# Kernel optimization log

Hardware: AMD Instinct MI355X
Metric: run time of the kernel (lower is better)

## Reference

```python
import jax, jax.numpy as jnp
import numpy as np

N_NODES = 100000
N_EDGES = 600000
NODE_DIM = 64
EDGE_DIM = 32
HID = 128
OUT = 24


def setup_inputs() -> dict:
    key = jax.random.key(0)
    ks = jax.random.split(key, 20)

    def w(k, shape):
        return jax.random.normal(k, shape, jnp.float32) * (1.0 / np.sqrt(shape[0]).astype(np.float32))

    inp = {}
    inp["x"] = jax.random.normal(ks[0], (N_NODES, NODE_DIM), jnp.float32)
    inp["edge_index"] = jax.random.randint(ks[1], (2, N_EDGES), 0, N_NODES)
    inp["edge_attr"] = jax.random.normal(ks[2], (N_EDGES, EDGE_DIM), jnp.float32)
    inp["lin1_w"] = w(ks[3], (NODE_DIM, HID)); inp["lin1_b"] = jnp.zeros((HID,), jnp.float32)
    i = 4
    for c in (1, 2, 3):
        inp[f"conv{c}_edge_w"] = w(ks[i], (EDGE_DIM, HID)); inp[f"conv{c}_edge_b"] = jnp.zeros((HID,), jnp.float32)
        inp[f"conv{c}_w1"] = w(ks[i + 1], (HID, HID)); inp[f"conv{c}_b1"] = jnp.zeros((HID,), jnp.float32)
        inp[f"conv{c}_w2"] = w(ks[i + 2], (HID, HID)); inp[f"conv{c}_b2"] = jnp.zeros((HID,), jnp.float32)
        i += 3
    inp["cls_w1"] = w(ks[i], (2 * HID + EDGE_DIM, HID)); inp["cls_b1"] = jnp.zeros((HID,), jnp.float32)
    inp["cls_w2"] = w(ks[i + 1], (HID, OUT)); inp["cls_b2"] = jnp.zeros((OUT,), jnp.float32)
    return inp


def _gine(h, src, dst, e_emb, w1, b1, w2, b2, eps=0.0):
    # GINEConv: out = MLP((1+eps)*x + sum_{j->i} relu(x_j + edge_emb))
    m = jax.nn.relu(h[src] + e_emb)                       # [E, HID] gather + fuse
    agg = jax.ops.segment_sum(m, dst, num_segments=N_NODES)  # scatter-add to dst
    z = (1.0 + eps) * h + agg
    return jax.nn.relu(z @ w1 + b1) @ w2 + b2


def reference(x, edge_index, edge_attr,
              lin1_w, lin1_b,
              conv1_edge_w, conv1_edge_b, conv1_w1, conv1_b1, conv1_w2, conv1_b2,
              conv2_edge_w, conv2_edge_b, conv2_w1, conv2_b1, conv2_w2, conv2_b2,
              conv3_edge_w, conv3_edge_b, conv3_w1, conv3_b1, conv3_w2, conv3_b2,
              cls_w1, cls_b1, cls_w2, cls_b2):
    src, dst = edge_index[0], edge_index[1]
    h = x @ lin1_w + lin1_b                               # [N, HID]
    layers = [
        (conv1_edge_w, conv1_edge_b, conv1_w1, conv1_b1, conv1_w2, conv1_b2),
        (conv2_edge_w, conv2_edge_b, conv2_w1, conv2_b1, conv2_w2, conv2_b2),
        (conv3_edge_w, conv3_edge_b, conv3_w1, conv3_b1, conv3_w2, conv3_b2),
    ]
    for ew, eb, w1, b1, w2, b2 in layers:
        e_emb = edge_attr @ ew + eb                       # [E, HID]
        h = jax.nn.relu(_gine(h, src, dst, e_emb, w1, b1, w2, b2))
    edge_feat = jnp.concatenate([h[src], h[dst], edge_attr], axis=-1)  # [E, 2*HID+EDGE_DIM]
    return jax.nn.relu(edge_feat @ cls_w1 + cls_b1) @ cls_w2 + cls_b2  # [E, OUT]
```

## Files before the change

### kernel.cpp

```cpp
#include <hip/hip_runtime.h>

#define N_NODES 100000
#define N_EDGES 600000
#define NODE_DIM 64
#define EDGE_DIM 32
#define HID 128
#define OUT_DIM 24

typedef short short8 __attribute__((ext_vector_type(8)));
typedef short short4v __attribute__((ext_vector_type(4)));
typedef float f32x4 __attribute__((ext_vector_type(4)));

#define MFMA16(a, b, c) __builtin_amdgcn_mfma_f32_16x16x32_bf16(a, b, c, 0, 0, 0)

__device__ inline unsigned short f2bf(float f) {
  unsigned u = __float_as_uint(f);
  u += 0x7FFFu + ((u >> 16) & 1u);
  return (unsigned short)(u >> 16);
}
__device__ inline float bf2f(unsigned short b) {
  return __uint_as_float(((unsigned)b) << 16);
}

#define OFF_CW1T 0
#define OFF_CW2T 36864
#define OFF_LAYER(c) (40960 + (c)*65536)
#define OFF_EWT(c) (237568 + (c)*8192)
#define W_TOTAL 262144

__global__ __launch_bounds__(256) void prep_weights(
    const float* __restrict__ cw1, const float* __restrict__ cw2,
    const float* __restrict__ l0w1, const float* __restrict__ l0w2,
    const float* __restrict__ l1w1, const float* __restrict__ l1w2,
    const float* __restrict__ l2w1, const float* __restrict__ l2w2,
    const float* __restrict__ e0w, const float* __restrict__ e1w,
    const float* __restrict__ e2w,
    unsigned short* __restrict__ wb) {
  int i = blockIdx.x * 256 + threadIdx.x;
  if (i < 36864) {
    int n = i / 288, k = i % 288;
    wb[OFF_CW1T + i] = f2bf(cw1[k * 128 + n]);
  }
  int j = i - 36864;
  if (j >= 0 && j < 4096) {
    int n = j / 128, k = j % 128;
    wb[OFF_CW2T + j] = f2bf(n < 24 ? cw2[k * 24 + n] : 0.f);
  }
  int t = i - 40960;
  if (t >= 0 && t < 3 * 32768) {
    int c = t / 32768, u = t % 32768;
    const float* w = (u < 16384) ? (c == 0 ? l0w1 : c == 1 ? l1w1 : l2w1)
                                 : (c == 0 ? l0w2 : c == 1 ? l1w2 : l2w2);
    int v = u & 16383;
    int n = v >> 7, k = v & 127;
    float val = w[k * 128 + n];
    unsigned short hi = f2bf(val);
    unsigned short lo = f2bf(val - bf2f(hi));
    int base = OFF_LAYER(c) + (u < 16384 ? 0 : 32768);
    wb[base + v] = hi;
    wb[base + 16384 + v] = lo;
  }
  int p = i - 139264;
  if (p >= 0 && p < 3 * 8192) {
    int c = p / 8192, u = p % 8192;
    int v = u & 4095;
    int s = v >> 3, jj = v & 7;
    int ntile = s >> 6, kgrp = (s >> 4) & 3, nrow = s & 15;
    int n = ntile * 16 + nrow, k = kgrp * 8 + jj;
    const float* ew = (c == 0 ? e0w : c == 1 ? e1w : e2w);
    float val = ew[k * 128 + n];
    unsigned short hi = f2bf(val);
    wb[OFF_EWT(c) + u] = (u < 4096) ? hi : f2bf(val - bf2f(hi));
  }
}

__global__ __launch_bounds__(256) void lin1_kernel(
    const float* __restrict__ x, const float* __restrict__ w,
    const float* __restrict__ b, float* __restrict__ h,
    unsigned short* __restrict__ hbf) {
  __shared__ float4 smem4[3072];
  float* sA = (float*)smem4;
  float* sB = (float*)smem4 + 4096;
  int tid = threadIdx.x;
  int tn = tid & 31, tm = tid >> 5;
  int mbase = blockIdx.x * 64;

  for (int i = tid; i < 1024; i += 256) {
    int m = i & 63, k4 = (i >> 6) << 2;
    int row = mbase + m; if (row >= N_NODES) row = N_NODES - 1;
    float4 v = *(const float4*)(x + (size_t)row * NODE_DIM + k4);
    sA[(k4 + 0) * 64 + m] = v.x; sA[(k4 + 1) * 64 + m] = v.y;
    sA[(k4 + 2) * 64 + m] = v.z; sA[(k4 + 3) * 64 + m] = v.w;
  }
  for (int i = tid; i < 2048; i += 256)
    *(float4*)&sB[i * 4] = ((const float4*)w)[i];
  __syncthreads();

  float acc[8][4] = {};
#pragma unroll 8
  for (int k = 0; k < 64; ++k) {
    float4 a0 = *(float4*)&sA[k * 64 + tm * 8];
    float4 a1 = *(float4*)&sA[k * 64 + tm * 8 + 4];
    float4 bv = *(float4*)&sB[k * 128 + tn * 4];
    float av[8] = {a0.x, a0.y, a0.z, a0.w, a1.x, a1.y, a1.z, a1.w};
    float bb[4] = {bv.x, bv.y, bv.z, bv.w};
#pragma unroll
    for (int i = 0; i < 8; ++i)
#pragma unroll
      for (int jj = 0; jj < 4; ++jj) acc[i][jj] = fmaf(av[i], bb[jj], acc[i][jj]);
  }
  float4 bv = *(const float4*)(b + tn * 4);
#pragma unroll
  for (int i = 0; i < 8; ++i) {
    int row = mbase + tm * 8 + i;
    if (row < N_NODES) {
      float4 o = {acc[i][0] + bv.x, acc[i][1] + bv.y, acc[i][2] + bv.z, acc[i][3] + bv.w};
      *(float4*)(h + (size_t)row * HID + tn * 4) = o;
      short4v pk = {(short)f2bf(o.x), (short)f2bf(o.y), (short)f2bf(o.z), (short)f2bf(o.w)};
      *(short4v*)(hbf + (size_t)row * HID + tn * 4) = pk;
    }
  }
}

__global__ __launch_bounds__(256) void hist_kernel(
    const int* __restrict__ dst, int* __restrict__ counts) {
  int e = blockIdx.x * 256 + threadIdx.x;
  if (e < N_EDGES) atomicAdd(&counts[dst[e]], 1);
}

#define SCAN_BLK 98
__global__ __launch_bounds__(256) void scan_partial(
    const int* __restrict__ cnt, int* __restrict__ partial) {
  __shared__ int sdata[256];
  int b = blockIdx.x, t = threadIdx.x;
  int sum = 0;
  for (int i = t; i < 1024; i += 256) {
    int idx = b * 1024 + i;
    sum += (idx < N_NODES) ? cnt[idx] : 0;
  }
  sdata[t] = sum; __syncthreads();
  for (int s = 128; s > 0; s >>= 1) {
    if (t < s) sdata[t] += sdata[t + s];
    __syncthreads();
  }
  if (t == 0) partial[b] = sdata[0];
}

__global__ void scan_sums(const int* __restrict__ partial,
                          int* __restrict__ partialScan, int* __restrict__ rowptr) {
  if (threadIdx.x == 0) {
    int acc = 0;
    for (int i = 0; i < SCAN_BLK; ++i) { partialScan[i] = acc; acc += partial[i]; }
    rowptr[N_NODES] = acc;
  }
}

__global__ __launch_bounds__(256) void scan_final(
    const int* __restrict__ cnt, const int* __restrict__ partialScan,
    int* __restrict__ rowptr, int* __restrict__ cur) {
  __shared__ int sdata[256];
  int b = blockIdx.x, t = threadIdx.x;
  int i0 = b * 1024 + t * 4;
  int c[4]; int s = 0;
#pragma unroll
  for (int j = 0; j < 4; ++j) {
    c[j] = (i0 + j < N_NODES) ? cnt[i0 + j] : 0;
    s += c[j];
  }
  sdata[t] = s; __syncthreads();
  for (int d = 1; d < 256; d <<= 1) {
    int u = (t >= d) ? sdata[t - d] : 0;
    __syncthreads();
    sdata[t] += u;
    __syncthreads();
  }
  int off = sdata[t] - s + partialScan[b];
#pragma unroll
  for (int j = 0; j < 4; ++j) {
    int idx = i0 + j;
    if (idx < N_NODES) { rowptr[idx] = off; cur[idx] = off; off += c[j]; }
  }
}

__global__ __launch_bounds__(256) void scatter_kernel(
    const int* __restrict__ dst, const int* __restrict__ src,
    int* __restrict__ cur, int* __restrict__ perm,
    int* __restrict__ srcp, int* __restrict__ dstp) {
  int e = blockIdx.x * 256 + threadIdx.x;
  if (e < N_EDGES) {
    int d = dst[e];
    int slot = atomicAdd(&cur[d], 1);
    perm[slot] = e;
    srcp[slot] = src[e];
    dstp[slot] = d;
  }
}

__global__ __launch_bounds__(256) void build_eafrag(
    const float* __restrict__ ea, const int* __restrict__ perm,
    unsigned short* __restrict__ frag) {
  int slot = blockIdx.x * 256 + threadIdx.x;
  if (slot >= N_EDGES) return;
  int e = perm[slot];
  const float4* row = (const float4*)(ea + (size_t)e * EDGE_DIM);
  unsigned short* dp = frag + ((size_t)(slot >> 7)) * 4096 +
                       (size_t)(((slot & 127) >> 4)) * 512 + (slot & 15) * 8;
#pragma unroll
  for (int kg = 0; kg < 4; ++kg) {
    float4 v0 = row[kg * 2], v1 = row[kg * 2 + 1];
    short8 pk = {(short)f2bf(v0.x), (short)f2bf(v0.y), (short)f2bf(v0.z), (short)f2bf(v0.w),
                 (short)f2bf(v1.x), (short)f2bf(v1.y), (short)f2bf(v1.z), (short)f2bf(v1.w)};
    *(short8*)(dp + kg * 128) = pk;
  }
}

__global__ __launch_bounds__(256) void edge_agg_kernel(
    const unsigned short* __restrict__ hbf, const unsigned short* __restrict__ eafrag,
    const int* __restrict__ srcp, const int* __restrict__ dstp,
    const unsigned short* __restrict__ ewt, const float* __restrict__ eb,
    float* __restrict__ agg) {
  __shared__ float emb[128 * 132];
  __shared__ int sidx[128];
  __shared__ int sdst[128];
  int tid = threadIdx.x, lane = tid & 63, wave = tid >> 6;
  int wm = wave & 1, wn = wave >> 1;
  int sbase = blockIdx.x * 128;
  int nrows = N_EDGES - sbase; if (nrows > 128) nrows = 128;
  if (tid < 128) {
    int sl = sbase + tid;
    sidx[tid] = (sl < N_EDGES) ? srcp[sl] : 0;
    sdst[tid] = (sl < N_EDGES) ? dstp[sl] : -1;
  }
  const short8* Af = (const short8*)(eafrag) + (size_t)blockIdx.x * 512;
  const short8* Bh = (const short8*)(ewt);
  const short8* Bl = (const short8*)(ewt + 4096);
  short8 af[4], bh[4], bl[4];
#pragma unroll
  for (int mt = 0; mt < 4; ++mt) af[mt] = Af[(wm * 4 + mt) * 64 + lane];
#pragma unroll
  for (int nt = 0; nt < 4; ++nt) {
    bh[nt] = Bh[(wn * 4 + nt) * 64 + lane];
    bl[nt] = Bl[(wn * 4 + nt) * 64 + lane];
  }
  const f32x4 zf = {0.f, 0.f, 0.f, 0.f};
  f32x4 acc[4][4];
#pragma unroll
  for (int mt = 0; mt < 4; ++mt)
#pragma unroll
    for (int nt = 0; nt < 4; ++nt) {
      acc[mt][nt] = MFMA16(af[mt], bh[nt], zf);
      acc[mt][nt] = MFMA16(af[mt], bl[nt], acc[mt][nt]);
    }
  int q = lane >> 4, r = lane & 15;
#pragma unroll
  for (int nt = 0; nt < 4; ++nt) {
    int n = wn * 64 + nt * 16 + r;
    float ebv = eb[n];
#pragma unroll
    for (int mt = 0; mt < 4; ++mt) {
      int rowb = (wm * 4 + mt) * 16 + q * 4;
#pragma unroll
      for (int i2 = 0; i2 < 4; ++i2)
        emb[(rowb + i2) * 132 + n] = acc[mt][nt][i2] + ebv;
    }
  }
  __syncthreads();
  {
    int r0 = wave * 32;
    int cl = (lane & 31) * 4;
#pragma unroll 8
    for (int rr = 0; rr < 16; ++rr) {
      int row = r0 + rr * 2 + (lane >> 5);
      int s = sidx[row];
      uint2 u = *(const uint2*)(hbf + (size_t)s * HID + cl);
      float4 ev = *(float4*)(emb + row * 132 + cl);
      ev.x = fmaxf(ev.x + bf2f((unsigned short)u.x), 0.f);
      ev.y = fmaxf(ev.y + bf2f((unsigned short)(u.x >> 16)), 0.f);
      ev.z = fmaxf(ev.z + bf2f((unsigned short)u.y), 0.f);
      ev.w = fmaxf(ev.w + bf2f((unsigned short)(u.y >> 16)), 0.f);
      *(float4*)(emb + row * 132 + cl) = ev;
    }
  }
  __syncthreads();
  {
    int hh = tid >> 7;
    int col = tid & 127;
    int rbeg = hh * 64;
    int rend = rbeg + 64; if (rend > nrows) rend = nrows;
    if (rbeg < rend) {
      float a = 0.f;
      int cnode = sdst[rbeg];
      bool atomic_first = true;
      for (int rr = rbeg; rr < rend; ++rr) {
        int node = sdst[rr];
        if (node != cnode) {
          if (atomic_first) atomicAdd(&agg[(size_t)cnode * HID + col], a);
          else agg[(size_t)cnode * HID + col] = a;
          a = 0.f; cnode = node; atomic_first = false;
        }
        a += emb[rr * 132 + col];
      }
      atomicAdd(&agg[(size_t)cnode * HID + col], a);
    }
  }
}

__global__ __launch_bounds__(256) void agg_gather_kernel(
    const float* __restrict__ h, const float* __restrict__ ea,
    const int* __restrict__ srcp, const int* __restrict__ perm,
    const int* __restrict__ rowptr,
    const float* __restrict__ ew, const float* __restrict__ eb,
    float* __restrict__ agg) {
  int tid = threadIdx.x, lane = tid & 63;
  int wid = blockIdx.x * 4 + (tid >> 6);
  int nwaves = gridDim.x * 4;
  const float2* ew2 = (const float2*)ew;
  float2 ebv = *(const float2*)(eb + lane * 2);

  for (int node = wid; node < N_NODES; node += nwaves) {
    int beg = rowptr[node], end = rowptr[node + 1];
    float2 acc = {0.f, 0.f};
    for (int i = beg; i < end; ++i) {
      int s0 = srcp[i];
      int e0 = perm[i];
      float2 h0 = *(const float2*)(h + (size_t)s0 * HID + lane * 2);
      const float4* ea0 = (const float4*)(ea + (size_t)e0 * EDGE_DIM);
      float2 m0 = ebv;
#pragma unroll
      for (int k4 = 0; k4 < 8; ++k4) {
        float4 a0 = ea0[k4];
        float a0v[4] = {a0.x, a0.y, a0.z, a0.w};
#pragma unroll
        for (int j = 0; j < 4; ++j) {
          float2 w = ew2[(k4 * 4 + j) * 64 + lane];
          m0.x = fmaf(a0v[j], w.x, m0.x);
          m0.y = fmaf(a0v[j], w.y, m0.y);
        }
      }
      acc.x += fmaxf(m0.x + h0.x, 0.f);
      acc.y += fmaxf(m0.y + h0.y, 0.f);
    }
    *(float2*)(agg + (size_t)node * HID + lane * 2) = acc;
  }
}

__global__ __launch_bounds__(256) void mlp_mfma(
    const float* __restrict__ h, const float* __restrict__ agg,
    const unsigned short* __restrict__ wl,
    const float* __restrict__ b1, const float* __restrict__ b2,
    float* __restrict__ hout, unsigned short* __restrict__ hbfout) {
  __shared__ unsigned short lds[40960];
  unsigned short* sAh = lds;
  unsigned short* sAl = lds + 4096;
  unsigned short* sBh = lds + 8192;
  unsigned short* sBl = lds + 12288;
  unsigned short* t1h = lds;
  unsigned short* t1l = lds + 16384;
  unsigned short* sB2h = lds + 32768;
  unsigned short* sB2l = lds + 36864;
  const unsigned short* w1h = wl;
  const unsigned short* w1l = wl + 16384;
  const unsigned short* w2h = wl + 32768;
  const unsigned short* w2l = wl + 49152;
  int tid = threadIdx.x, lane = tid & 63, wave = tid >> 6;
  int wm = wave & 1, wn = wave >> 1;
  int mbase = blockIdx.x * 128;
  const f32x4 zf = {0.f, 0.f, 0.f, 0.f};

  f32x4 acc[4][4];
#pragma unroll
  for (int a = 0; a < 4; ++a)
#pragma unroll
    for (int bq = 0; bq < 4; ++bq) acc[a][bq] = zf;

  for (int c = 0; c < 4; ++c) {
    __syncthreads();
#pragma unroll
    for (int it = 0; it < 4; ++it) {
      int idx = it * 256 + tid;
      int m = idx >> 3, k4 = (idx & 7) * 4;
      int row = mbase + m; if (row >= N_NODES) row = N_NODES - 1;
      size_t g = (size_t)row * HID + c * 32 + k4;
      float4 hv = *(const float4*)(h + g);
      float4 av = *(const float4*)(agg + g);
      float z0 = hv.x + av.x, z1 = hv.y + av.y, z2 = hv.z + av.z, z3 = hv.w + av.w;
      unsigned short h0 = f2bf(z0), h1 = f2bf(z1), h2 = f2bf(z2), h3 = f2bf(z3);
      int slot = ((m >> 4) * 4 + (k4 >> 3)) * 16 + (m & 15);
      int off = slot * 8 + (k4 & 7);
      short4v ph = {(short)h0, (short)h1, (short)h2, (short)h3};
      short4v pl = {(short)f2bf(z0 - bf2f(h0)), (short)f2bf(z1 - bf2f(h1)),
                    (short)f2bf(z2 - bf2f(h2)), (short)f2bf(z3 - bf2f(h3))};
      *(short4v*)(sAh + off) = ph;
      *(short4v*)(sAl + off) = pl;
    }
#pragma unroll
    for (int it = 0; it < 2; ++it) {
      int s = it * 256 + tid;
      int ntile = s >> 6, kgrp = (s >> 4) & 3, nrow = s & 15;
      int goff = (ntile * 16 + nrow) * 128 + c * 32 + kgrp * 8;
      *(short8*)(sBh + s * 8) = *(const short8*)(w1h + goff);
      *(short8*)(sBl + s * 8) = *(const short8*)(w1l + goff);
    }
    __syncthreads();
    short8 ah[4], al[4], bh[4], bl[4];
#pragma unroll
    for (int mt = 0; mt < 4; ++mt) {
      ah[mt] = *(short8*)(sAh + ((wm * 4 + mt) * 64 + lane) * 8);
      al[mt] = *(short8*)(sAl + ((wm * 4 + mt) * 64 + lane) * 8);
    }
#pragma unroll
    for (int nt = 0; nt < 4; ++nt) {
      bh[nt] = *(short8*)(sBh + ((wn * 4 + nt) * 64 + lane) * 8);
      bl[nt] = *(short8*)(sBl + ((wn * 4 + nt) * 64 + lane) * 8);
    }
#pragma unroll
    for (int mt = 0; mt < 4; ++mt)
#pragma unroll
      for (int nt = 0; nt < 4; ++nt) {
        acc[mt][nt] = MFMA16(ah[mt], bh[nt], acc[mt][nt]);
        acc[mt][nt] = MFMA16(ah[mt], bl[nt], acc[mt][nt]);
        acc[mt][nt] = MFMA16(al[mt], bh[nt], acc[mt][nt]);
      }
  }
  __syncthreads();
  int q = lane >> 4, r = lane & 15;
#pragma unroll
  for (int nt = 0; nt < 4; ++nt) {
    int n = wn * 64 + nt * 16 + r;
    float b1v = b1[n];
    int kgrp = n >> 3, jj = n & 7;
#pragma unroll
    for (int mt = 0; mt < 4; ++mt) {
      int mtg = wm * 4 + mt;
#pragma unroll
      for (int i2 = 0; i2 < 4; ++i2) {
        int mrow = q * 4 + i2;
        float val = fmaxf(acc[mt][nt][i2] + b1v, 0.f);
        unsigned short hi = f2bf(val);
        int idx = ((mtg * 16 + kgrp) * 16 + mrow) * 8 + jj;
        t1h[idx] = hi;
        t1l[idx] = f2bf(val - bf2f(hi));
      }
    }
  }

  f32x4 acc2[4][4];
#pragma unroll
  for (int a = 0; a < 4; ++a)
#pragma unroll
    for (int bq = 0; bq < 4; ++bq) acc2[a][bq] = zf;

  for (int kc = 0; kc < 4; ++kc) {
    __syncthreads();
#pragma unroll
    for (int it = 0; it < 2; ++it) {
      int s = it * 256 + tid;
      int ntile = s >> 6, kgrp = (s >> 4) & 3, nrow = s & 15;
      int goff = (ntile * 16 + nrow) * 128 + kc * 32 + kgrp * 8;
      *(short8*)(sB2h + s * 8) = *(const short8*)(w2h + goff);
      *(short8*)(sB2l + s * 8) = *(const short8*)(w2l + goff);
    }
    __syncthreads();
    short8 ah[4], al[4], bh[4], bl[4];
#pragma unroll
    for (int mt = 0; mt < 4; ++mt) {
      int mtg = wm * 4 + mt;
      int idx = ((mtg * 16 + kc * 4 + q) * 16 + r) * 8;
      ah[mt] = *(short8*)(t1h + idx);
      al[mt] = *(short8*)(t1l + idx);
    }
#pragma unroll
    for (int nt = 0; nt < 4; ++nt) {
      bh[nt] = *(short8*)(sB2h + ((wn * 4 + nt) * 64 + lane) * 8);
      bl[nt] = *(short8*)(sB2l + ((wn * 4 + nt) * 64 + lane) * 8);
    }
#pragma unroll
    for (int mt = 0; mt < 4; ++mt)
#pragma unroll
      for (int nt = 0; nt < 4; ++nt) {
        acc2[mt][nt] = MFMA16(ah[mt], bh[nt], acc2[mt][nt]);
        acc2[mt][nt] = MFMA16(ah[mt], bl[nt], acc2[mt][nt]);
        acc2[mt][nt] = MFMA16(al[mt], bh[nt], acc2[mt][nt]);
      }
  }
#pragma unroll
  for (int nt = 0; nt < 4; ++nt) {
    int n = wn * 64 + nt * 16 + r;
    float b2v = b2[n];
#pragma unroll
    for (int mt = 0; mt < 4; ++mt) {
      int mtg = wm * 4 + mt;
#pragma unroll
      for (int i2 = 0; i2 < 4; ++i2) {
        int row = mbase + mtg * 16 + q * 4 + i2;
        if (row < N_NODES) {
          float val = fmaxf(acc2[mt][nt][i2] + b2v, 0.f);
          hout[(size_t)row * HID + n] = val;
          hbfout[(size_t)row * HID + n] = f2bf(val);
        }
      }
    }
  }
}

__global__ __launch_bounds__(256) void cls_mfma(
    const unsigned short* __restrict__ hbf, const float* __restrict__ ea,
    const int* __restrict__ src, const int* __restrict__ dst,
    const unsigned short* __restrict__ w1t, const unsigned short* __restrict__ w2t,
    const float* __restrict__ b1, const float* __restrict__ b2,
    float* __restrict__ out) {
  __shared__ unsigned short lds[20480];
  unsigned short* sA2 = lds;
  unsigned short* sBp = lds + 8192;
  unsigned short* t1 = lds;
  unsigned short* sB2 = lds + 16384;
  __shared__ int sidx[256];
  int tid = threadIdx.x, lane = tid & 63, wave = tid >> 6;
  int wm = wave & 1, wn = wave >> 1;
  int q = lane >> 4, r = lane & 15;
  int ebase = blockIdx.x * 128;
  const f32x4 zf = {0.f, 0.f, 0.f, 0.f};

  {
    int e0 = ebase + (tid & 127);
    if (e0 >= N_EDGES) e0 = N_EDGES - 1;
    sidx[tid] = (tid < 128 ? src : dst)[e0];
  }

  f32x4 acc[4][4];
#pragma unroll
  for (int a = 0; a < 4; ++a)
#pragma unroll
    for (int bq = 0; bq < 4; ++bq) acc[a][bq] = zf;

  for (int cp = 0; cp < 4; ++cp) {
    __syncthreads();
#pragma unroll
    for (int it = 0; it < 4; ++it) {
      int idx = it * 256 + tid;
      int m = idx >> 3, sub = idx & 7;
      int node = (cp < 2) ? sidx[m] : sidx[128 + m];
      int eoff = (cp & 1) * 64;
      short8 v = *(const short8*)(hbf + (size_t)node * HID + eoff + sub * 8);
      int ch = sub >> 2, kg = sub & 3;
      *(short8*)(sA2 + ch * 4096 +
                 (((m >> 4) * 4 + kg) * 16 + ((m & 15) ^ sub)) * 8) = v;
    }
#pragma unroll
    for (int it = 0; it < 4; ++it) {
      int s2 = it * 256 + tid;
      int ch = s2 >> 9, s = s2 & 511;
      int ntile = s >> 6, kgrp = (s >> 4) & 3, nrow = s & 15;
      int c = cp * 2 + ch;
      *(short8*)(sBp + ch * 4096 + s * 8) =
          *(const short8*)(w1t + (ntile * 16 + nrow) * 288 + c * 32 + kgrp * 8);
    }
    __syncthreads();
#pragma unroll
    for (int ch = 0; ch < 2; ++ch) {
      short8 af[4], bfv[4];
#pragma unroll
      for (int mt = 0; mt < 4; ++mt)
        af[mt] = *(short8*)(sA2 + ch * 4096 +
                            (((wm * 4 + mt) * 4 + q) * 16 + (r ^ (ch * 4 + q))) * 8);
#pragma unroll
      for (int nt = 0; nt < 4; ++nt)
        bfv[nt] = *(short8*)(sBp + ch * 4096 + ((wn * 4 + nt) * 64 + lane) * 8);
#pragma unroll
      for (int mt = 0; mt < 4; ++mt)
#pragma unroll
        for (int nt = 0; nt < 4; ++nt)
          acc[mt][nt] = MFMA16(af[mt], bfv[nt], acc[mt][nt]);
    }
  }
  __syncthreads();
#pragma unroll
  for (int it = 0; it < 4; ++it) {
    int idx = it * 256 + tid;
    int m = idx >> 3, k4 = (idx & 7) * 4;
    int e8 = ebase + m; if (e8 >= N_EDGES) e8 = N_EDGES - 1;
    float4 v = *(const float4*)(ea + (size_t)e8 * EDGE_DIM + k4);
    int kg = k4 >> 3;
    int slot = ((m >> 4) * 4 + kg) * 16 + ((m & 15) ^ kg);
    short4v pk = {(short)f2bf(v.x), (short)f2bf(v.y), (short)f2bf(v.z), (short)f2bf(v.w)};
    *(short4v*)(sA2 + slot * 8 + (k4 & 7)) = pk;
  }
#pragma unroll
  for (int it = 0; it < 2; ++it) {
    int s = it * 256 + tid;
    int ntile = s >> 6, kgrp = (s >> 4) & 3, nrow = s & 15;
    *(short8*)(sBp + s * 8) =
        *(const short8*)(w1t + (ntile * 16 + nrow) * 288 + 8 * 32 + kgrp * 8);
  }
  __syncthreads();
  {
    short8 af[4], bfv[4];
#pragma unroll
    for (int mt = 0; mt < 4; ++mt)
      af[mt] = *(short8*)(sA2 + (((wm * 4 + mt) * 4 + q) * 16 + (r ^ q)) * 8);
#pragma unroll
    for (int nt = 0; nt < 4; ++nt)
      bfv[nt] = *(short8*)(sBp + ((wn * 4 + nt) * 64 + lane) * 8);
#pragma unroll
    for (int mt = 0; mt < 4; ++mt)
#pragma unroll
      for (int nt = 0; nt < 4; ++nt)
        acc[mt][nt] = MFMA16(af[mt], bfv[nt], acc[mt][nt]);
  }
  __syncthreads();
#pragma unroll
  for (int nt = 0; nt < 4; ++nt) {
    int n = wn * 64 + nt * 16 + r;
    float b1v = b1[n];
    int kgrp = n >> 3, jj = n & 7;
#pragma unroll
    for (int mt = 0; mt < 4; ++mt) {
      int mtg = wm * 4 + mt;
#pragma unroll
      for (int i2 = 0; i2 < 4; ++i2) {
        int mrow = q * 4 + i2;
        float val = fmaxf(acc[mt][nt][i2] + b1v, 0.f);
        t1[((mtg * 16 + kgrp) * 16 + mrow) * 8 + jj] = f2bf(val);
      }
    }
  }
#pragma unroll
  for (int it = 0; it < 2; ++it) {
    int s = it * 256 + tid;
    int ntile = s >> 8, kgrp = (s >> 4) & 15, nrow = s & 15;
    *(short8*)(sB2 + s * 8) = *(const short8*)(w2t + (ntile * 16 + nrow) * 128 + kgrp * 8);
  }
  __syncthreads();

  f32x4 acc2[2][2];
  acc2[0][0] = zf; acc2[0][1] = zf; acc2[1][0] = zf; acc2[1][1] = zf;
#pragma unroll
  for (int kc = 0; kc < 4; ++kc) {
    short8 a0 = *(short8*)(t1 + (((wave * 2 + 0) * 16 + kc * 4 + q) * 16 + r) * 8);
    short8 a1 = *(short8*)(t1 + (((wave * 2 + 1) * 16 + kc * 4 + q) * 16 + r) * 8);
    short8 b0 = *(short8*)(sB2 + ((0 * 16 + kc * 4 + q) * 16 + r) * 8);
    short8 b1f = *(short8*)(sB2 + ((1 * 16 + kc * 4 + q) * 16 + r) * 8);
    acc2[0][0] = MFMA16(a0, b0, acc2[0][0]);
    acc2[0][1] = MFMA16(a0, b1f, acc2[0][1]);
    acc2[1][0] = MFMA16(a1, b0, acc2[1][0]);
    acc2[1][1] = MFMA16(a1, b1f, acc2[1][1]);
  }
#pragma unroll
  for (int nt2 = 0; nt2 < 2; ++nt2) {
    int n = nt2 * 16 + r;
    float b2v = (n < OUT_DIM) ? b2[n] : 0.f;
#pragma unroll
    for (int mt2 = 0; mt2 < 2; ++mt2) {
      int mtg = wave * 2 + mt2;
#pragma unroll
      for (int i2 = 0; i2 < 4; ++i2) {
        int e = ebase + mtg * 16 + q * 4 + i2;
        if (n < OUT_DIM && e < N_EDGES)
          out[(size_t)e * OUT_DIM + n] = acc2[mt2][nt2][i2] + b2v;
      }
    }
  }
}

extern "C" void kernel_launch(void* const* d_in, const int* in_sizes, int n_in,
                              void* d_out, int out_size, void* d_ws, size_t ws_size,
                              hipStream_t stream) {
  const float* x = (const float*)d_in[0];
  const int* ei = (const int*)d_in[1];
  const float* ea = (const float*)d_in[2];
  const float* lin1_w = (const float*)d_in[3];
  const float* lin1_b = (const float*)d_in[4];
  const int* src = ei;
  const int* dst = ei + N_EDGES;

  const size_t NH = (size_t)N_NODES * HID;
  float* bufA = (float*)d_ws;
  float* bufB = bufA + NH;
  int* ibase = (int*)(bufB + NH);
  int* rowptr = ibase;
  int* cur = ibase + 100004;
  int* counts = ibase + 200004;
  int* perm = ibase + 300004;
  int* partial = ibase + 900004;
  int* partialScan = ibase + 900132;
  int* srcp = ibase + 900260;
  int* dstp = ibase + 1500260;
  unsigned short* hbf = (unsigned short*)(ibase + 2100264);
  unsigned short* eafrag = hbf + (size_t)N_NODES * HID;
  size_t need = (size_t)((char*)(eafrag + (size_t)N_EDGES * EDGE_DIM) - (char*)d_ws) +
                (size_t)W_TOTAL * 2 + 4096;
  bool big = ws_size >= need;
  unsigned short* wbase = (unsigned short*)((((uintptr_t)d_ws + ws_size) - (size_t)W_TOTAL * 2) & ~(uintptr_t)255);

  prep_weights<<<(163840 + 255) / 256, 256, 0, stream>>>(
      (const float*)d_in[23], (const float*)d_in[25],
      (const float*)d_in[7], (const float*)d_in[9],
      (const float*)d_in[13], (const float*)d_in[15],
      (const float*)d_in[19], (const float*)d_in[21],
      (const float*)d_in[5], (const float*)d_in[11], (const float*)d_in[17],
      wbase);

  lin1_kernel<<<(N_NODES + 63) / 64, 256, 0, stream>>>(x, lin1_w, lin1_b, bufA, hbf);

  hipMemsetAsync(counts, 0, N_NODES * sizeof(int), stream);
  hist_kernel<<<(N_EDGES + 255) / 256, 256, 0, stream>>>(dst, counts);
  scan_partial<<<SCAN_BLK, 256, 0, stream>>>(counts, partial);
  scan_sums<<<1, 64, 0, stream>>>(partial, partialScan, rowptr);
  scan_final<<<SCAN_BLK, 256, 0, stream>>>(counts, partialScan, rowptr, cur);
  scatter_kernel<<<(N_EDGES + 255) / 256, 256, 0, stream>>>(dst, src, cur, perm, srcp, dstp);
  if (big)
    build_eafrag<<<(N_EDGES + 255) / 256, 256, 0, stream>>>(ea, perm, eafrag);

  float* hcur = bufA;
  float* aux = bufB;
  for (int c = 0; c < 3; ++c) {
    const float* ew = (const float*)d_in[5 + c * 6 + 0];
    const float* eb = (const float*)d_in[5 + c * 6 + 1];
    const float* b1 = (const float*)d_in[5 + c * 6 + 3];
    const float* b2 = (const float*)d_in[5 + c * 6 + 5];
    if (big) {
      hipMemsetAsync(aux, 0, NH * sizeof(float), stream);
      edge_agg_kernel<<<(N_EDGES + 127) / 128, 256, 0, stream>>>(
          hbf, eafrag, srcp, dstp, wbase + OFF_EWT(c), eb, aux);
    } else {
      agg_gather_kernel<<<2048, 256, 0, stream>>>(
          hcur, ea, srcp, perm, rowptr, ew, eb, aux);
    }
    mlp_mfma<<<(N_NODES + 127) / 128, 256, 0, stream>>>(
        hcur, aux, wbase + OFF_LAYER(c), b1, b2, aux, hbf);
    float* tmp = hcur; hcur = aux; aux = tmp;
  }

  const float* cb1 = (const float*)d_in[24];
  const float* cb2 = (const float*)d_in[26];
  cls_mfma<<<(N_EDGES + 127) / 128, 256, 0, stream>>>(
      hbf, ea, src, dst, wbase + OFF_CW1T, wbase + OFF_CW2T, cb1, cb2, (float*)d_out);
}
```

Measured before the change: 985.1 us.

## Prefetch gathers into registers and read MFMA-fragment weights directly from global

The classifier weights are now stored in MFMA fragment order, so cls_mfma loads B operands straight from global memory instead of staging them through LDS. The gathered node rows are double-buffered in LDS with a register prefetch of the next chunk, which removes one barrier per chunk and overlaps the gather with the MFMAs. The edge aggregation kernel issues all 16 h[src] gathers before the edge-embedding MFMA so that gather latency overlaps the compute. The cost is more register pressure, plus B-operand reads that now rely on cache hits.

```diff
diff --git a/kernel.cpp b/kernel.cpp
--- a/kernel.cpp
+++ b/kernel.cpp
@@ -38,12 +38,20 @@
     unsigned short* __restrict__ wb) {
   int i = blockIdx.x * 256 + threadIdx.x;
   if (i < 36864) {
-    int n = i / 288, k = i % 288;
+    int c = i >> 12, v = i & 4095;
+    int f = v >> 3, jj = v & 7;
+    int t = f >> 6, l = f & 63;
+    int n = t * 16 + (l & 15);
+    int k = c * 32 + (l >> 4) * 8 + jj;
     wb[OFF_CW1T + i] = f2bf(cw1[k * 128 + n]);
   }
   int j = i - 36864;
   if (j >= 0 && j < 4096) {
-    int n = j / 128, k = j % 128;
+    int f = j >> 3, jj = j & 7;
+    int nt2 = f >> 8, rem = f & 255;
+    int kc = rem >> 6, l = rem & 63;
+    int n = nt2 * 16 + (l & 15);
+    int k = kc * 32 + (l >> 4) * 8 + jj;
     wb[OFF_CW2T + j] = f2bf(n < 24 ? cw2[k * 24 + n] : 0.f);
   }
   int t = i - 40960;
@@ -231,6 +239,17 @@
     sidx[tid] = (sl < N_EDGES) ? srcp[sl] : 0;
     sdst[tid] = (sl < N_EDGES) ? dstp[sl] : -1;
   }
+  __syncthreads();
+
+  int r0 = wave * 32;
+  int cl = (lane & 31) * 4;
+  uint2 g[16];
+#pragma unroll
+  for (int rr = 0; rr < 16; ++rr) {
+    int row = r0 + rr * 2 + (lane >> 5);
+    g[rr] = *(const uint2*)(hbf + (size_t)sidx[row] * HID + cl);
+  }
+
   const short8* Af = (const short8*)(eafrag) + (size_t)blockIdx.x * 512;
   const short8* Bh = (const short8*)(ewt);
   const short8* Bl = (const short8*)(ewt + 4096);
@@ -265,21 +284,16 @@
     }
   }
   __syncthreads();
-  {
-    int r0 = wave * 32;
-    int cl = (lane & 31) * 4;
-#pragma unroll 8
-    for (int rr = 0; rr < 16; ++rr) {
-      int row = r0 + rr * 2 + (lane >> 5);
-      int s = sidx[row];
-      uint2 u = *(const uint2*)(hbf + (size_t)s * HID + cl);
-      float4 ev = *(float4*)(emb + row * 132 + cl);
-      ev.x = fmaxf(ev.x + bf2f((unsigned short)u.x), 0.f);
-      ev.y = fmaxf(ev.y + bf2f((unsigned short)(u.x >> 16)), 0.f);
-      ev.z = fmaxf(ev.z + bf2f((unsigned short)u.y), 0.f);
-      ev.w = fmaxf(ev.w + bf2f((unsigned short)(u.y >> 16)), 0.f);
-      *(float4*)(emb + row * 132 + cl) = ev;
-    }
+#pragma unroll
+  for (int rr = 0; rr < 16; ++rr) {
+    int row = r0 + rr * 2 + (lane >> 5);
+    float4 ev = *(float4*)(emb + row * 132 + cl);
+    uint2 u = g[rr];
+    ev.x = fmaxf(ev.x + bf2f((unsigned short)u.x), 0.f);
+    ev.y = fmaxf(ev.y + bf2f((unsigned short)(u.x >> 16)), 0.f);
+    ev.z = fmaxf(ev.z + bf2f((unsigned short)u.y), 0.f);
+    ev.w = fmaxf(ev.w + bf2f((unsigned short)(u.y >> 16)), 0.f);
+    *(float4*)(emb + row * 132 + cl) = ev;
   }
   __syncthreads();
   {
@@ -506,14 +520,11 @@
 __global__ __launch_bounds__(256) void cls_mfma(
     const unsigned short* __restrict__ hbf, const float* __restrict__ ea,
     const int* __restrict__ src, const int* __restrict__ dst,
-    const unsigned short* __restrict__ w1t, const unsigned short* __restrict__ w2t,
+    const unsigned short* __restrict__ w1f, const unsigned short* __restrict__ w2f,
     const float* __restrict__ b1, const float* __restrict__ b2,
     float* __restrict__ out) {
-  __shared__ unsigned short lds[20480];
-  unsigned short* sA2 = lds;
-  unsigned short* sBp = lds + 8192;
+  __shared__ unsigned short lds[16384];
   unsigned short* t1 = lds;
-  unsigned short* sB2 = lds + 16384;
   __shared__ int sidx[256];
   int tid = threadIdx.x, lane = tid & 63, wave = tid >> 6;
   int wm = wave & 1, wn = wave >> 1;
@@ -526,6 +537,7 @@
     if (e0 >= N_EDGES) e0 = N_EDGES - 1;
     sidx[tid] = (tid < 128 ? src : dst)[e0];
   }
+  __syncthreads();
 
   f32x4 acc[4][4];
 #pragma unroll
@@ -533,39 +545,54 @@
 #pragma unroll
     for (int bq = 0; bq < 4; ++bq) acc[a][bq] = zf;
 
+  int sub = tid & 7, mb = tid >> 3;
+  int ch = sub >> 2, kg = sub & 3;
+
+  short8 pf[4];
+#pragma unroll
+  for (int it = 0; it < 4; ++it) {
+    int m = it * 32 + mb;
+    pf[it] = *(const short8*)(hbf + (size_t)sidx[m] * HID + sub * 8);
+  }
+  float4 ef[4];
+
   for (int cp = 0; cp < 4; ++cp) {
-    __syncthreads();
+    unsigned short* bufA = lds + (cp & 1) * 8192;
 #pragma unroll
     for (int it = 0; it < 4; ++it) {
-      int idx = it * 256 + tid;
-      int m = idx >> 3, sub = idx & 7;
-      int node = (cp < 2) ? sidx[m] : sidx[128 + m];
-      int eoff = (cp & 1) * 64;
-      short8 v = *(const short8*)(hbf + (size_t)node * HID + eoff + sub * 8);
-      int ch = sub >> 2, kg = sub & 3;
-      *(short8*)(sA2 + ch * 4096 +
-                 (((m >> 4) * 4 + kg) * 16 + ((m & 15) ^ sub)) * 8) = v;
-    }
-#pragma unroll
-    for (int it = 0; it < 4; ++it) {
-      int s2 = it * 256 + tid;
-      int ch = s2 >> 9, s = s2 & 511;
-      int ntile = s >> 6, kgrp = (s >> 4) & 3, nrow = s & 15;
-      int c = cp * 2 + ch;
-      *(short8*)(sBp + ch * 4096 + s * 8) =
-          *(const short8*)(w1t + (ntile * 16 + nrow) * 288 + c * 32 + kgrp * 8);
-    }
-    __syncthreads();
-#pragma unroll
-    for (int ch = 0; ch < 2; ++ch) {
+      int m = it * 32 + mb;
+      *(short8*)(bufA + ch * 4096 +
+                 (((m >> 4) * 4 + kg) * 16 + ((m & 15) ^ sub)) * 8) = pf[it];
+    }
+    if (cp < 3) {
+      int ncp = cp + 1;
+      int eoff = (ncp & 1) * 64;
+#pragma unroll
+      for (int it = 0; it < 4; ++it) {
+        int m = it * 32 + mb;
+        int node = (ncp < 2) ? sidx[m] : sidx[128 + m];
+        pf[it] = *(const short8*)(hbf + (size_t)node * HID + eoff + sub * 8);
+      }
+    } else {
+#pragma unroll
+      for (int it = 0; it < 4; ++it) {
+        int m = it * 32 + mb;
+        int e8 = ebase + m; if (e8 >= N_EDGES) e8 = N_EDGES - 1;
+        ef[it] = *(const float4*)(ea + (size_t)e8 * EDGE_DIM + sub * 4);
+      }
+    }
+    __syncthreads();
+#pragma unroll
+    for (int ch2 = 0; ch2 < 2; ++ch2) {
+      int c = cp * 2 + ch2;
       short8 af[4], bfv[4];
 #pragma unroll
+      for (int nt = 0; nt < 4; ++nt)
+        bfv[nt] = *(const short8*)(w1f + (size_t)c * 4096 + ((wn * 4 + nt) * 64 + lane) * 8);
+#pragma unroll
       for (int mt = 0; mt < 4; ++mt)
-        af[mt] = *(short8*)(sA2 + ch * 4096 +
-                            (((wm * 4 + mt) * 4 + q) * 16 + (r ^ (ch * 4 + q))) * 8);
-#pragma unroll
-      for (int nt = 0; nt < 4; ++nt)
-        bfv[nt] = *(short8*)(sBp + ch * 4096 + ((wn * 4 + nt) * 64 + lane) * 8);
+        af[mt] = *(short8*)(bufA + ch2 * 4096 +
+                            (((wm * 4 + mt) * 4 + q) * 16 + (r ^ (ch2 * 4 + q))) * 8);
 #pragma unroll
       for (int mt = 0; mt < 4; ++mt)
 #pragma unroll
@@ -573,34 +600,25 @@
           acc[mt][nt] = MFMA16(af[mt], bfv[nt], acc[mt][nt]);
     }
   }
-  __syncthreads();
-#pragma unroll
-  for (int it = 0; it < 4; ++it) {
-    int idx = it * 256 + tid;
-    int m = idx >> 3, k4 = (idx & 7) * 4;
-    int e8 = ebase + m; if (e8 >= N_EDGES) e8 = N_EDGES - 1;
-    float4 v = *(const float4*)(ea + (size_t)e8 * EDGE_DIM + k4);
-    int kg = k4 >> 3;
-    int slot = ((m >> 4) * 4 + kg) * 16 + ((m & 15) ^ kg);
-    short4v pk = {(short)f2bf(v.x), (short)f2bf(v.y), (short)f2bf(v.z), (short)f2bf(v.w)};
-    *(short4v*)(sA2 + slot * 8 + (k4 & 7)) = pk;
-  }
-#pragma unroll
-  for (int it = 0; it < 2; ++it) {
-    int s = it * 256 + tid;
-    int ntile = s >> 6, kgrp = (s >> 4) & 3, nrow = s & 15;
-    *(short8*)(sBp + s * 8) =
-        *(const short8*)(w1t + (ntile * 16 + nrow) * 288 + 8 * 32 + kgrp * 8);
-  }
-  __syncthreads();
   {
+    unsigned short* bufA = lds;
+    int k4 = sub * 4, kgE = k4 >> 3;
+#pragma unroll
+    for (int it = 0; it < 4; ++it) {
+      int m = it * 32 + mb;
+      float4 v = ef[it];
+      int slot = ((m >> 4) * 4 + kgE) * 16 + ((m & 15) ^ kgE);
+      short4v pk = {(short)f2bf(v.x), (short)f2bf(v.y), (short)f2bf(v.z), (short)f2bf(v.w)};
+      *(short4v*)(bufA + slot * 8 + (k4 & 7)) = pk;
+    }
+    __syncthreads();
     short8 af[4], bfv[4];
 #pragma unroll
+    for (int nt = 0; nt < 4; ++nt)
+      bfv[nt] = *(const short8*)(w1f + (size_t)8 * 4096 + ((wn * 4 + nt) * 64 + lane) * 8);
+#pragma unroll
     for (int mt = 0; mt < 4; ++mt)
-      af[mt] = *(short8*)(sA2 + (((wm * 4 + mt) * 4 + q) * 16 + (r ^ q)) * 8);
-#pragma unroll
-    for (int nt = 0; nt < 4; ++nt)
-      bfv[nt] = *(short8*)(sBp + ((wn * 4 + nt) * 64 + lane) * 8);
+      af[mt] = *(short8*)(bufA + (((wm * 4 + mt) * 4 + q) * 16 + (r ^ q)) * 8);
 #pragma unroll
     for (int mt = 0; mt < 4; ++mt)
 #pragma unroll
@@ -624,12 +642,6 @@
       }
     }
   }
-#pragma unroll
-  for (int it = 0; it < 2; ++it) {
-    int s = it * 256 + tid;
-    int ntile = s >> 8, kgrp = (s >> 4) & 15, nrow = s & 15;
-    *(short8*)(sB2 + s * 8) = *(const short8*)(w2t + (ntile * 16 + nrow) * 128 + kgrp * 8);
-  }
   __syncthreads();
 
   f32x4 acc2[2][2];
@@ -638,8 +650,8 @@
   for (int kc = 0; kc < 4; ++kc) {
     short8 a0 = *(short8*)(t1 + (((wave * 2 + 0) * 16 + kc * 4 + q) * 16 + r) * 8);
     short8 a1 = *(short8*)(t1 + (((wave * 2 + 1) * 16 + kc * 4 + q) * 16 + r) * 8);
-    short8 b0 = *(short8*)(sB2 + ((0 * 16 + kc * 4 + q) * 16 + r) * 8);
-    short8 b1f = *(short8*)(sB2 + ((1 * 16 + kc * 4 + q) * 16 + r) * 8);
+    short8 b0 = *(const short8*)(w2f + (kc * 64 + lane) * 8);
+    short8 b1f = *(const short8*)(w2f + (256 + kc * 64 + lane) * 8);
     acc2[0][0] = MFMA16(a0, b0, acc2[0][0]);
     acc2[0][1] = MFMA16(a0, b1f, acc2[0][1]);
     acc2[1][0] = MFMA16(a1, b0, acc2[1][0]);
```

Result: faster. 917.7 us (-6.8%).
